# Performance work log

Measured on AMD Instinct MI355X. Metric: run time of the kernel, lower is better.

## Reference

```python
import jax, jax.numpy as jnp
import numpy as np

CTX = 1024   # context_window
D = 512      # emb_dim
B = 8        # batch


def make_rotary_matrix(ctx, d):
    """Dense block-diagonal RoPE rotation matrices R: [ctx, d, d]."""
    pos = jnp.arange(ctx, dtype=jnp.float32)[:, None]          # [ctx, 1]
    i = jnp.arange(d // 2, dtype=jnp.float32)                  # [d/2]
    theta = pos / (10000.0 ** (2.0 * i / d))                   # [ctx, d/2]
    cos, sin = jnp.cos(theta), jnp.sin(theta)
    idx = jnp.arange(d // 2)
    R = jnp.zeros((ctx, d, d), jnp.float32)
    R = R.at[:, 2 * idx, 2 * idx].set(cos)
    R = R.at[:, 2 * idx, 2 * idx + 1].set(-sin)
    R = R.at[:, 2 * idx + 1, 2 * idx].set(sin)
    R = R.at[:, 2 * idx + 1, 2 * idx + 1].set(cos)
    return R


def setup_inputs() -> dict:
    key = jax.random.key(0)
    ks = jax.random.split(key, 8)
    s = 1.0 / np.sqrt(D)
    inp = {
        "x": jax.random.normal(ks[0], (B, CTX, D), jnp.float32),
        "w_q": jax.random.uniform(ks[1], (D, D), jnp.float32, -s, s),
        "b_q": jax.random.uniform(ks[2], (D,), jnp.float32, -s, s),
        "w_k": jax.random.uniform(ks[3], (D, D), jnp.float32, -s, s),
        "b_k": jax.random.uniform(ks[4], (D,), jnp.float32, -s, s),
        "w_v": jax.random.uniform(ks[5], (D, D), jnp.float32, -s, s),
        "b_v": jax.random.uniform(ks[6], (D,), jnp.float32, -s, s),
        "R": make_rotary_matrix(CTX, D),
        "kv_cache": 0,  # bool flag; does not affect output
    }
    return inp


def reference(x, w_q, b_q, w_k, b_k, w_v, b_v, R, kv_cache):
    B_, C, Dm = x.shape
    q = x @ w_q.T + b_q                      # [B, C, D]
    k = x @ w_k.T + b_k
    v = x @ w_v.T + b_v
    Rc = R[:C]                               # [C, D, D]
    # torch.bmm(q.transpose(0,1), R.transpose(1,2)).transpose(0,1)
    # out[b,c,e] = sum_d q[b,c,d] * R[c,e,d]
    q_rot = jnp.einsum("bcd,ced->bce", q, Rc)
    k_rot = jnp.einsum("bcd,ced->bce", k, Rc)
    # causal SDPA (eval mode: dropout omitted)
    scale = 1.0 / jnp.sqrt(jnp.asarray(Dm, jnp.float32))
    scores = jnp.einsum("bqe,bke->bqk", q_rot, k_rot) * scale   # [B, C, C]
    causal = jnp.tril(jnp.ones((C, C), bool))
    scores = jnp.where(causal, scores, jnp.finfo(scores.dtype).min)
    attn = jax.nn.softmax(scores, axis=-1)
    return jnp.einsum("bqk,bkd->bqd", attn, v)
```

## Files before the change

### kernel.cpp

```cpp
#include <hip/hip_runtime.h>

#define BATCH 8
#define CTXN  1024
#define DMODEL 512

using short8  = __attribute__((ext_vector_type(8))) short;
using f32x16  = __attribute__((ext_vector_type(16))) float;

typedef const void __attribute__((address_space(1)))* as1_cvp;
typedef void __attribute__((address_space(3)))* as3_vp;

__device__ __forceinline__ unsigned short f2bf(float f) {
  unsigned int u = __float_as_uint(f);
  u += 0x7fffu + ((u >> 16) & 1u);
  return (unsigned short)(u >> 16);
}

#define X4  1048576
#define W4  65536
#define CAST_BLOCKS 4864
__global__ __launch_bounds__(256) void prep_all(const float* __restrict__ x,
                                                const float* __restrict__ wq,
                                                const float* __restrict__ wk,
                                                const float* __restrict__ wv,
                                                unsigned short* __restrict__ xb,
                                                unsigned short* __restrict__ wb,
                                                float2* __restrict__ tab) {
  if (blockIdx.x < CAST_BLOCKS) {
    int gid = blockIdx.x * 256 + threadIdx.x;
    const float4* src; ushort4* dst;
    if (gid < X4)                { src = (const float4*)x  + gid;              dst = (ushort4*)xb + gid; }
    else if (gid < X4 + W4)      { int o = gid - X4;        src = (const float4*)wq + o; dst = (ushort4*)wb + o; }
    else if (gid < X4 + 2 * W4)  { int o = gid - X4 - W4;   src = (const float4*)wk + o; dst = (ushort4*)(wb + 262144) + o; }
    else                         { int o = gid - X4 - 2*W4; src = (const float4*)wv + o; dst = (ushort4*)(wb + 524288) + o; }
    float4 f = *src;
    ushort4 u;
    u.x = f2bf(f.x); u.y = f2bf(f.y); u.z = f2bf(f.z); u.w = f2bf(f.w);
    *dst = u;
  } else {
    int c = blockIdx.x - CAST_BLOCKS;
    int i = threadIdx.x;
    float freq = exp2f((float)i * (-13.287712379549449f / 256.0f));
    float th = (float)c * freq;
    float sn, cs;
    sincosf(th, &sn, &cs);
    tab[c * 256 + i] = make_float2(cs, sn);
  }
}

__device__ __forceinline__ void issue_tile(const unsigned short* __restrict__ gA, int ldA,
                                           const unsigned short* __restrict__ gB, int ldB,
                                           unsigned short* sA, unsigned short* sB,
                                           int slot, int tid) {
  unsigned short* dA = sA + (slot << 13);
  unsigned short* dB = sB + (slot << 13);
#pragma unroll
  for (int c = 0; c < 2; ++c) {
    int li  = (c << 9) + tid;
    int row = li >> 3;
    int ch  = (li & 7) ^ (row & 7);
    __builtin_amdgcn_global_load_lds((as1_cvp)(gA + (size_t)row * ldA + (ch << 3)),
                                     (as3_vp)(dA + (li << 3)), 16, 0, 0);
  }
#pragma unroll
  for (int c = 0; c < 2; ++c) {
    int li  = (c << 9) + tid;
    int row = li >> 3;
    int ch  = (li & 7) ^ (row & 7);
    __builtin_amdgcn_global_load_lds((as1_cvp)(gB + (size_t)row * ldB + (ch << 3)),
                                     (as3_vp)(dB + (li << 3)), 16, 0, 0);
  }
}

__device__ __forceinline__ void gemm_pipe(const unsigned short* __restrict__ gA, int ldA,
                                          const unsigned short* __restrict__ gB, int ldB,
                                          int nt, unsigned short* sA, unsigned short* sB,
                                          int tid, f32x16 acc[2]) {
  const int l = tid & 63, w = tid >> 6, wr = w >> 2, wc = w & 3;
  const int cl = l & 31, hi = l >> 5;
  int aoff[2][4], boff[4];
#pragma unroll
  for (int m = 0; m < 2; ++m) {
    int ra = wr * 64 + m * 32 + cl;
#pragma unroll
    for (int ks = 0; ks < 4; ++ks) {
      int kc = ks * 2 + hi;
      aoff[m][ks] = ra * 64 + ((kc ^ (ra & 7)) << 3);
    }
  }
  {
    int rb = wc * 32 + cl;
#pragma unroll
    for (int ks = 0; ks < 4; ++ks) {
      int kc = ks * 2 + hi;
      boff[ks] = rb * 64 + ((kc ^ (rb & 7)) << 3);
    }
  }
  issue_tile(gA, ldA, gB, ldB, sA, sB, 0, tid);
  issue_tile(gA + 64, ldA, gB + 64, ldB, sA, sB, 1, tid);
  asm volatile("s_waitcnt vmcnt(4)" ::: "memory");
  __builtin_amdgcn_s_barrier();
  __builtin_amdgcn_sched_barrier(0);

  for (int t = 0; t < nt; ++t) {
    const unsigned short* sAb = sA + ((t & 1) << 13);
    const unsigned short* sBb = sB + ((t & 1) << 13);
    short8 af[2][4], bfv[4];
    af[0][0] = *(const short8*)(sAb + aoff[0][0]);
    af[1][0] = *(const short8*)(sAb + aoff[1][0]);
    bfv[0]   = *(const short8*)(sBb + boff[0]);
#pragma unroll
    for (int ks = 0; ks < 3; ++ks) {
      af[0][ks + 1] = *(const short8*)(sAb + aoff[0][ks + 1]);
      af[1][ks + 1] = *(const short8*)(sAb + aoff[1][ks + 1]);
      bfv[ks + 1]   = *(const short8*)(sBb + boff[ks + 1]);
      asm volatile("s_waitcnt lgkmcnt(3)" ::: "memory");
      __builtin_amdgcn_sched_barrier(0);
      __builtin_amdgcn_s_setprio(1);
      acc[0] = __builtin_amdgcn_mfma_f32_32x32x16_bf16(af[0][ks], bfv[ks], acc[0], 0, 0, 0);
      acc[1] = __builtin_amdgcn_mfma_f32_32x32x16_bf16(af[1][ks], bfv[ks], acc[1], 0, 0, 0);
      __builtin_amdgcn_s_setprio(0);
    }
    asm volatile("s_waitcnt lgkmcnt(0)" ::: "memory");
    __builtin_amdgcn_sched_barrier(0);
    __builtin_amdgcn_s_barrier();
    if (t + 2 < nt) {
      issue_tile(gA + (size_t)(t + 2) * 64, ldA, gB + (size_t)(t + 2) * 64, ldB, sA, sB, t & 1, tid);
      asm volatile("s_waitcnt vmcnt(4)" ::: "memory");
    } else {
      asm volatile("s_waitcnt vmcnt(0)" ::: "memory");
    }
    __builtin_amdgcn_sched_barrier(0);
    __builtin_amdgcn_s_setprio(1);
    acc[0] = __builtin_amdgcn_mfma_f32_32x32x16_bf16(af[0][3], bfv[3], acc[0], 0, 0, 0);
    acc[1] = __builtin_amdgcn_mfma_f32_32x32x16_bf16(af[1][3], bfv[3], acc[1], 0, 0, 0);
    __builtin_amdgcn_s_setprio(0);
    __builtin_amdgcn_s_barrier();
    __builtin_amdgcn_sched_barrier(0);
  }
}

__device__ __forceinline__ void issue_tile64(const unsigned short* __restrict__ gA, int ldA,
                                             const unsigned short* __restrict__ gB, int ldB,
                                             unsigned short* sA, unsigned short* sB,
                                             int slot, int tid) {
  unsigned short* dA = sA + (slot << 12);
  unsigned short* dB = sB + (slot << 13);
#pragma unroll
  for (int c = 0; c < 2; ++c) {
    int li  = (c << 8) + tid;
    int row = li >> 3;
    int ch  = (li & 7) ^ (row & 7);
    __builtin_amdgcn_global_load_lds((as1_cvp)(gA + (size_t)row * ldA + (ch << 3)),
                                     (as3_vp)(dA + (li << 3)), 16, 0, 0);
  }
#pragma unroll
  for (int c = 0; c < 4; ++c) {
    int li  = (c << 8) + tid;
    int row = li >> 3;
    int ch  = (li & 7) ^ (row & 7);
    __builtin_amdgcn_global_load_lds((as1_cvp)(gB + (size_t)row * ldB + (ch << 3)),
                                     (as3_vp)(dB + (li << 3)), 16, 0, 0);
  }
}

__device__ __forceinline__ void gemm_pipe64(const unsigned short* __restrict__ gA, int ldA,
                                            const unsigned short* __restrict__ gB, int ldB,
                                            int nt, unsigned short* sA, unsigned short* sB,
                                            int tid, f32x16 acc[2]) {
  const int l = tid & 63, w = tid >> 6;
  const int cl = l & 31, hi = l >> 5;
  int aoff[2][4], boff[4];
#pragma unroll
  for (int m = 0; m < 2; ++m) {
    int ra = m * 32 + cl;
#pragma unroll
    for (int ks = 0; ks < 4; ++ks) {
      int kc = ks * 2 + hi;
      aoff[m][ks] = ra * 64 + ((kc ^ (ra & 7)) << 3);
    }
  }
  {
    int rb = w * 32 + cl;
#pragma unroll
    for (int ks = 0; ks < 4; ++ks) {
      int kc = ks * 2 + hi;
      boff[ks] = rb * 64 + ((kc ^ (rb & 7)) << 3);
    }
  }
  issue_tile64(gA, ldA, gB, ldB, sA, sB, 0, tid);
  issue_tile64(gA + 64, ldA, gB + 64, ldB, sA, sB, 1, tid);
  asm volatile("s_waitcnt vmcnt(6)" ::: "memory");
  __builtin_amdgcn_s_barrier();
  __builtin_amdgcn_sched_barrier(0);

  for (int t = 0; t < nt; ++t) {
    const unsigned short* sAb = sA + ((t & 1) << 12);
    const unsigned short* sBb = sB + ((t & 1) << 13);
    short8 af[2][4], bfv[4];
    af[0][0] = *(const short8*)(sAb + aoff[0][0]);
    af[1][0] = *(const short8*)(sAb + aoff[1][0]);
    bfv[0]   = *(const short8*)(sBb + boff[0]);
#pragma unroll
    for (int ks = 0; ks < 3; ++ks) {
      af[0][ks + 1] = *(const short8*)(sAb + aoff[0][ks + 1]);
      af[1][ks + 1] = *(const short8*)(sAb + aoff[1][ks + 1]);
      bfv[ks + 1]   = *(const short8*)(sBb + boff[ks + 1]);
      asm volatile("s_waitcnt lgkmcnt(3)" ::: "memory");
      __builtin_amdgcn_sched_barrier(0);
      __builtin_amdgcn_s_setprio(1);
      acc[0] = __builtin_amdgcn_mfma_f32_32x32x16_bf16(af[0][ks], bfv[ks], acc[0], 0, 0, 0);
      acc[1] = __builtin_amdgcn_mfma_f32_32x32x16_bf16(af[1][ks], bfv[ks], acc[1], 0, 0, 0);
      __builtin_amdgcn_s_setprio(0);
    }
    asm volatile("s_waitcnt lgkmcnt(0)" ::: "memory");
    __builtin_amdgcn_sched_barrier(0);
    __builtin_amdgcn_s_barrier();
    if (t + 2 < nt) {
      issue_tile64(gA + (size_t)(t + 2) * 64, ldA, gB + (size_t)(t + 2) * 64, ldB, sA, sB, t & 1, tid);
      asm volatile("s_waitcnt vmcnt(6)" ::: "memory");
    } else {
      asm volatile("s_waitcnt vmcnt(0)" ::: "memory");
    }
    __builtin_amdgcn_sched_barrier(0);
    __builtin_amdgcn_s_setprio(1);
    acc[0] = __builtin_amdgcn_mfma_f32_32x32x16_bf16(af[0][3], bfv[3], acc[0], 0, 0, 0);
    acc[1] = __builtin_amdgcn_mfma_f32_32x32x16_bf16(af[1][3], bfv[3], acc[1], 0, 0, 0);
    __builtin_amdgcn_s_setprio(0);
    __builtin_amdgcn_s_barrier();
    __builtin_amdgcn_sched_barrier(0);
  }
}


__global__ __launch_bounds__(512, 4) void qkv_kernel(const unsigned short* __restrict__ xb,
                                                     const unsigned short* __restrict__ wb,
                                                     const float* __restrict__ bq,
                                                     const float* __restrict__ bk,
                                                     const float* __restrict__ bv,
                                                     const float2* __restrict__ tab,
                                                     unsigned short* __restrict__ qrot,
                                                     unsigned short* __restrict__ krot,
                                                     unsigned short* __restrict__ vt) {
  __shared__ __align__(16) unsigned short sA[2 * 8192];
  __shared__ __align__(16) unsigned short sB[2 * 8192];
  int t = threadIdx.x, w = t >> 6, l = t & 63, wr = w >> 2, wc = w & 3;
  int cl = l & 31, hi = l >> 5;
  int m0 = blockIdx.x * 128, n0 = blockIdx.y * 128;
  f32x16 acc[2] = {};
  gemm_pipe(xb + (size_t)m0 * 512, 512, wb + (size_t)n0 * 512, 512, 8, sA, sB, t, acc);

  int sec = n0 >> 9;
  const float* bias = (sec == 0) ? bq : (sec == 1) ? bk : bv;
  unsigned short* qk_dst = (sec == 0) ? qrot : krot;
  int e = (n0 + wc * 32 + cl) & 511;
  float bsv = bias[e];
  if (sec < 2) {
    int i2 = e >> 1;
#pragma unroll
    for (int m = 0; m < 2; ++m) {
      int rowb = m0 + wr * 64 + m * 32 + 4 * hi;
#pragma unroll
      for (int r = 0; r < 16; ++r) {
        int mg = rowb + (r & 3) + 8 * (r >> 2);
        int cpos = mg & (CTXN - 1);
        float val  = acc[m][r] + bsv;
        float part = __shfl_xor(val, 1);
        float2 cs  = tab[cpos * 256 + i2];
        float o = (e & 1) ? fmaf(part, cs.y, val * cs.x)
                          : fmaf(-part, cs.y, val * cs.x);
        qk_dst[(size_t)mg * 512 + e] = f2bf(o);
      }
    }
  } else {
#pragma unroll
    for (int m = 0; m < 2; ++m) {
      int rowb0 = m0 + wr * 64 + m * 32 + 4 * hi;
#pragma unroll
      for (int q = 0; q < 4; ++q) {
        int rowb = rowb0 + 8 * q;
        int bidx = rowb >> 10;
        int cpos = rowb & (CTXN - 1);
        ushort4 pk;
        pk.x = f2bf(acc[m][q * 4 + 0] + bsv);
        pk.y = f2bf(acc[m][q * 4 + 1] + bsv);
        pk.z = f2bf(acc[m][q * 4 + 2] + bsv);
        pk.w = f2bf(acc[m][q * 4 + 3] + bsv);
        *(ushort4*)(vt + ((size_t)bidx * 512 + e) * 1024 + cpos) = pk;
      }
    }
  }
}

__device__ const unsigned char T64_IT[72] = {
  0,1,2,2,3,3,4,4,4,5,5,5,6,6,6,6,7,7,7,7,
  8,8,8,8,8,9,9,9,9,9,10,10,10,10,10,10,11,11,11,11,11,11,
  12,12,12,12,12,12,12,13,13,13,13,13,13,13,
  14,14,14,14,14,14,14,14,15,15,15,15,15,15,15,15};
__device__ const unsigned char T64_JT[72] = {
  0,0,0,1,0,1,0,1,2,0,1,2,0,1,2,3,0,1,2,3,
  0,1,2,3,4,0,1,2,3,4,0,1,2,3,4,5,0,1,2,3,4,5,
  0,1,2,3,4,5,6,0,1,2,3,4,5,6,
  0,1,2,3,4,5,6,7,0,1,2,3,4,5,6,7};

__global__ __launch_bounds__(256, 3) void scores_kernel(const unsigned short* __restrict__ qr,
                                                        const unsigned short* __restrict__ kr,
                                                        unsigned short* __restrict__ P,
                                                        float* __restrict__ lsum) {
  int it = T64_IT[blockIdx.x], jt = T64_JT[blockIdx.x], b = blockIdx.y;
  __shared__ __align__(16) unsigned short sA[2 * 4096];
  __shared__ __align__(16) unsigned short sB[2 * 8192];
  int t = threadIdx.x, w = t >> 6, l = t & 63;
  int cl = l & 31, hi = l >> 5;
  const unsigned short* A  = qr + ((size_t)b << 19) + (size_t)it * 64 * 512;
  const unsigned short* Bp = kr + ((size_t)b << 19) + (size_t)jt * 128 * 512;
  f32x16 acc[2] = {};
  gemm_pipe64(A, 512, Bp, 512, 8, sA, sB, t, acc);

  const float scale = 0.04419417382415922f;
  unsigned short* Pb = P + ((size_t)b << 20);
  float* lb = lsum + b * 1024;
  int j = jt * 128 + w * 32 + cl;
#pragma unroll
  for (int m = 0; m < 2; ++m) {
    int iqb = it * 64 + m * 32 + 4 * hi;
#pragma unroll
    for (int r = 0; r < 16; ++r) {
      int row = iqb + (r & 3) + 8 * (r >> 2);
      float p = (j <= row) ? __expf(acc[m][r] * scale) : 0.0f;
      Pb[(size_t)row * 1024 + j] = f2bf(p);
      float sp = p;
      sp += __shfl_xor(sp, 1);  sp += __shfl_xor(sp, 2);  sp += __shfl_xor(sp, 4);
      sp += __shfl_xor(sp, 8);  sp += __shfl_xor(sp, 16);
      if (cl == 0) atomicAdd(&lb[row], sp);
    }
  }
}

__global__ __launch_bounds__(256, 3) void pv_kernel(const unsigned short* __restrict__ P,
                                                    const unsigned short* __restrict__ vt,
                                                    const float* __restrict__ lsum,
                                                    float* __restrict__ out) {
  int it = blockIdx.x, nt2 = blockIdx.y, b = blockIdx.z;
  __shared__ __align__(16) unsigned short sA[2 * 4096];
  __shared__ __align__(16) unsigned short sB[2 * 8192];
  int t = threadIdx.x, w = t >> 6, l = t & 63;
  int cl = l & 31, hi = l >> 5;
  const unsigned short* A  = P  + ((size_t)b << 20) + (size_t)it * 64 * 1024;
  const unsigned short* Bp = vt + ((size_t)b << 19) + (size_t)nt2 * 128 * 1024;
  int nt = ((it >> 1) + 1) * 2;
  f32x16 acc[2] = {};
  gemm_pipe64(A, 1024, Bp, 1024, nt, sA, sB, t, acc);

  float* ob = out + ((size_t)b << 19);
  const float* lb = lsum + b * 1024;
  int d = nt2 * 128 + w * 32 + cl;
#pragma unroll
  for (int m = 0; m < 2; ++m) {
    int iqb = it * 64 + m * 32 + 4 * hi;
#pragma unroll
    for (int r = 0; r < 16; ++r) {
      int row = iqb + (r & 3) + 8 * (r >> 2);
      ob[(size_t)row * 512 + d] = acc[m][r] * (1.0f / lb[row]);
    }
  }
}

extern "C" void kernel_launch(void* const* d_in, const int* in_sizes, int n_in,
                              void* d_out, int out_size, void* d_ws, size_t ws_size,
                              hipStream_t stream) {
  const float* x  = (const float*)d_in[0];
  const float* wq = (const float*)d_in[1];
  const float* bq = (const float*)d_in[2];
  const float* wk = (const float*)d_in[3];
  const float* bk = (const float*)d_in[4];
  const float* wv = (const float*)d_in[5];
  const float* bv = (const float*)d_in[6];
  float* out = (float*)d_out;

  char* ws = (char*)d_ws;
  float2*         tab  = (float2*)(ws);
  unsigned short* xb   = (unsigned short*)(ws + (2ull  << 20));
  unsigned short* wb   = (unsigned short*)(ws + (10ull << 20));
  unsigned short* qrot = (unsigned short*)(ws + (12ull << 20));
  unsigned short* krot = (unsigned short*)(ws + (20ull << 20));
  unsigned short* vt   = (unsigned short*)(ws + (28ull << 20));
  unsigned short* P    = (unsigned short*)(ws + (36ull << 20));
  float*          lsum = (float*)(ws + (52ull << 20));

  hipMemsetAsync(lsum, 0, BATCH * CTXN * sizeof(float), stream);
  prep_all<<<dim3(CAST_BLOCKS + CTXN), dim3(256), 0, stream>>>(x, wq, wk, wv, xb, wb, tab);
  qkv_kernel<<<dim3(64, 12), dim3(512), 0, stream>>>(xb, wb, bq, bk, bv, tab, qrot, krot, vt);
  scores_kernel<<<dim3(72, BATCH), dim3(256), 0, stream>>>(qrot, krot, P, lsum);
  pv_kernel<<<dim3(16, 4, BATCH), dim3(256), 0, stream>>>(P, vt, lsum, out);
}
```

Measured before the change: 79.98 us.

## Compute softmax row sums in PV kernel from LDS tiles instead of atomics

Removes the shuffle-reduction and atomicAdd row-sum accumulation from the scores kernel, along with the memset of the lsum buffer. The PV kernel now sums the bf16 P values it already stages in shared memory each k-step, then reduces the partial sums through shared memory before normalising. This drops the global atomics and one memset launch, but adds extra LDS reads and ALU work inside the PV main loop. Row sums now come from the bf16-rounded P, which matches the numerator more consistently.

After: 69.14 us. 13.6% less time.

```diff
diff --git a/kernel.cpp b/kernel.cpp
--- a/kernel.cpp
+++ b/kernel.cpp
@@ -14,6 +14,9 @@
   unsigned int u = __float_as_uint(f);
   u += 0x7fffu + ((u >> 16) & 1u);
   return (unsigned short)(u >> 16);
+}
+__device__ __forceinline__ float bf2f(unsigned short u) {
+  return __uint_as_float((unsigned int)u << 16);
 }
 
 #define X4  1048576
@@ -164,10 +167,11 @@
   }
 }
 
+template <bool RSUM>
 __device__ __forceinline__ void gemm_pipe64(const unsigned short* __restrict__ gA, int ldA,
                                             const unsigned short* __restrict__ gB, int ldB,
                                             int nt, unsigned short* sA, unsigned short* sB,
-                                            int tid, f32x16 acc[2]) {
+                                            int tid, f32x16 acc[2], float* lacc) {
   const int l = tid & 63, w = tid >> 6;
   const int cl = l & 31, hi = l >> 5;
   int aoff[2][4], boff[4];
@@ -188,6 +192,11 @@
       boff[ks] = rb * 64 + ((kc ^ (rb & 7)) << 3);
     }
   }
+  const int srow = tid >> 2;
+  const int kc0  = (tid & 3) * 2;
+  const int soff0 = srow * 64 + (((kc0)     ^ (srow & 7)) << 3);
+  const int soff1 = srow * 64 + (((kc0 + 1) ^ (srow & 7)) << 3);
+
   issue_tile64(gA, ldA, gB, ldB, sA, sB, 0, tid);
   issue_tile64(gA + 64, ldA, gB + 64, ldB, sA, sB, 1, tid);
   asm volatile("s_waitcnt vmcnt(6)" ::: "memory");
@@ -197,7 +206,7 @@
   for (int t = 0; t < nt; ++t) {
     const unsigned short* sAb = sA + ((t & 1) << 12);
     const unsigned short* sBb = sB + ((t & 1) << 13);
-    short8 af[2][4], bfv[4];
+    short8 af[2][4], bfv[4], sr0, sr1;
     af[0][0] = *(const short8*)(sAb + aoff[0][0]);
     af[1][0] = *(const short8*)(sAb + aoff[1][0]);
     bfv[0]   = *(const short8*)(sBb + boff[0]);
@@ -213,6 +222,10 @@
       acc[1] = __builtin_amdgcn_mfma_f32_32x32x16_bf16(af[1][ks], bfv[ks], acc[1], 0, 0, 0);
       __builtin_amdgcn_s_setprio(0);
     }
+    if (RSUM) {
+      sr0 = *(const short8*)(sAb + soff0);
+      sr1 = *(const short8*)(sAb + soff1);
+    }
     asm volatile("s_waitcnt lgkmcnt(0)" ::: "memory");
     __builtin_amdgcn_sched_barrier(0);
     __builtin_amdgcn_s_barrier();
@@ -223,6 +236,12 @@
       asm volatile("s_waitcnt vmcnt(0)" ::: "memory");
     }
     __builtin_amdgcn_sched_barrier(0);
+    if (RSUM) {
+      float ls = 0.0f;
+#pragma unroll
+      for (int j = 0; j < 8; ++j) ls += bf2f((unsigned short)sr0[j]) + bf2f((unsigned short)sr1[j]);
+      *lacc += ls;
+    }
     __builtin_amdgcn_s_setprio(1);
     acc[0] = __builtin_amdgcn_mfma_f32_32x32x16_bf16(af[0][3], bfv[3], acc[0], 0, 0, 0);
     acc[1] = __builtin_amdgcn_mfma_f32_32x32x16_bf16(af[1][3], bfv[3], acc[1], 0, 0, 0);
@@ -305,8 +324,7 @@
 
 __global__ __launch_bounds__(256, 3) void scores_kernel(const unsigned short* __restrict__ qr,
                                                         const unsigned short* __restrict__ kr,
-                                                        unsigned short* __restrict__ P,
-                                                        float* __restrict__ lsum) {
+                                                        unsigned short* __restrict__ P) {
   int it = T64_IT[blockIdx.x], jt = T64_JT[blockIdx.x], b = blockIdx.y;
   __shared__ __align__(16) unsigned short sA[2 * 4096];
   __shared__ __align__(16) unsigned short sB[2 * 8192];
@@ -315,11 +333,11 @@
   const unsigned short* A  = qr + ((size_t)b << 19) + (size_t)it * 64 * 512;
   const unsigned short* Bp = kr + ((size_t)b << 19) + (size_t)jt * 128 * 512;
   f32x16 acc[2] = {};
-  gemm_pipe64(A, 512, Bp, 512, 8, sA, sB, t, acc);
+  float dummy = 0.0f;
+  gemm_pipe64<false>(A, 512, Bp, 512, 8, sA, sB, t, acc, &dummy);
 
   const float scale = 0.04419417382415922f;
   unsigned short* Pb = P + ((size_t)b << 20);
-  float* lb = lsum + b * 1024;
   int j = jt * 128 + w * 32 + cl;
 #pragma unroll
   for (int m = 0; m < 2; ++m) {
@@ -329,39 +347,41 @@
       int row = iqb + (r & 3) + 8 * (r >> 2);
       float p = (j <= row) ? __expf(acc[m][r] * scale) : 0.0f;
       Pb[(size_t)row * 1024 + j] = f2bf(p);
-      float sp = p;
-      sp += __shfl_xor(sp, 1);  sp += __shfl_xor(sp, 2);  sp += __shfl_xor(sp, 4);
-      sp += __shfl_xor(sp, 8);  sp += __shfl_xor(sp, 16);
-      if (cl == 0) atomicAdd(&lb[row], sp);
     }
   }
 }
 
 __global__ __launch_bounds__(256, 3) void pv_kernel(const unsigned short* __restrict__ P,
                                                     const unsigned short* __restrict__ vt,
-                                                    const float* __restrict__ lsum,
                                                     float* __restrict__ out) {
   int it = blockIdx.x, nt2 = blockIdx.y, b = blockIdx.z;
   __shared__ __align__(16) unsigned short sA[2 * 4096];
   __shared__ __align__(16) unsigned short sB[2 * 8192];
+  __shared__ float lpart[64][4];
+  __shared__ float lsum[64];
   int t = threadIdx.x, w = t >> 6, l = t & 63;
   int cl = l & 31, hi = l >> 5;
   const unsigned short* A  = P  + ((size_t)b << 20) + (size_t)it * 64 * 1024;
   const unsigned short* Bp = vt + ((size_t)b << 19) + (size_t)nt2 * 128 * 1024;
   int nt = ((it >> 1) + 1) * 2;
   f32x16 acc[2] = {};
-  gemm_pipe64(A, 1024, Bp, 1024, nt, sA, sB, t, acc);
+  float lacc = 0.0f;
+  gemm_pipe64<true>(A, 1024, Bp, 1024, nt, sA, sB, t, acc, &lacc);
+
+  lpart[t >> 2][t & 3] = lacc;
+  __syncthreads();
+  if (t < 64) lsum[t] = (lpart[t][0] + lpart[t][1]) + (lpart[t][2] + lpart[t][3]);
+  __syncthreads();
 
   float* ob = out + ((size_t)b << 19);
-  const float* lb = lsum + b * 1024;
   int d = nt2 * 128 + w * 32 + cl;
 #pragma unroll
   for (int m = 0; m < 2; ++m) {
-    int iqb = it * 64 + m * 32 + 4 * hi;
+    int rl0 = m * 32 + 4 * hi;
 #pragma unroll
     for (int r = 0; r < 16; ++r) {
-      int row = iqb + (r & 3) + 8 * (r >> 2);
-      ob[(size_t)row * 512 + d] = acc[m][r] * (1.0f / lb[row]);
+      int rl = rl0 + (r & 3) + 8 * (r >> 2);
+      ob[(size_t)(it * 64 + rl) * 512 + d] = acc[m][r] * (1.0f / lsum[rl]);
     }
   }
 }
@@ -386,11 +406,9 @@
   unsigned short* krot = (unsigned short*)(ws + (20ull << 20));
   unsigned short* vt   = (unsigned short*)(ws + (28ull << 20));
   unsigned short* P    = (unsigned short*)(ws + (36ull << 20));
-  float*          lsum = (float*)(ws + (52ull << 20));
-
-  hipMemsetAsync(lsum, 0, BATCH * CTXN * sizeof(float), stream);
+
   prep_all<<<dim3(CAST_BLOCKS + CTXN), dim3(256), 0, stream>>>(x, wq, wk, wv, xb, wb, tab);
   qkv_kernel<<<dim3(64, 12), dim3(512), 0, stream>>>(xb, wb, bq, bk, bv, tab, qrot, krot, vt);
-  scores_kernel<<<dim3(72, BATCH), dim3(256), 0, stream>>>(qrot, krot, P, lsum);
-  pv_kernel<<<dim3(16, 4, BATCH), dim3(256), 0, stream>>>(P, vt, lsum, out);
-}
+  scores_kernel<<<dim3(72, BATCH), dim3(256), 0, stream>>>(qrot, krot, P);
+  pv_kernel<<<dim3(16, 4, BATCH), dim3(256), 0, stream>>>(P, vt, out);
+}
```
